# Kernel tuning notes

Measured on AMD Instinct MI355X. Metric: run time of the kernel, lower is better.

Reference implementation:

```python
import jax, jax.numpy as jnp
import numpy as np

CAPSULES = 64
CAPSULE_DIM = 32
ROUTINGS = 3
EPS = 1e-7  # K.epsilon()


def setup_inputs() -> dict:
    key = jax.random.key(0)
    k1, k2 = jax.random.split(key)
    inputs = jax.random.normal(k1, (32, 2048, 16), dtype=jnp.float32)
    # W: (capsules, input_capsules, capsule_dim, input_capsule_dim), glorot-ish scale
    W = jax.random.normal(k2, (CAPSULES, 2048, CAPSULE_DIM, 16), dtype=jnp.float32) * 0.05
    return {"inputs": inputs, "W": W}


def squash(s):
    # s: [..., capsule_dim]
    s_norm = jnp.sum(jnp.square(s), axis=-1, keepdims=True)
    scale = s_norm / (1.0 + s_norm) / jnp.sqrt(s_norm + EPS)
    return s * scale


def reference(inputs, W):
    # inputs: [b, i, j] (batch, input_capsules, input_capsule_dim)
    # W:      [c, i, d, j] (capsules, input_capsules, capsule_dim, input_capsule_dim)
    # u_hat = batched predictions: [b, c, i, d]
    u_hat = jnp.einsum('bij,cidj->bcid', inputs, W)
    B = inputs.shape[0]
    b = jnp.zeros((B, CAPSULES, u_hat.shape[2]), dtype=u_hat.dtype)
    v = None
    for r in range(ROUTINGS):
        c = jax.nn.softmax(b, axis=1)              # softmax over capsules axis
        s = jnp.einsum('bci,bcid->bcd', c, u_hat)  # weighted sum over input capsules
        v = squash(s)                              # [b, c, d]
        # Original updates b for r > 0; the update at the final iteration has no
        # effect on the output, so it is skipped for efficiency (identical math).
        if 0 < r < ROUTINGS - 1:
            b = b + jnp.einsum('bcd,bcid->bci', v, u_hat)
    return v
```

## Files before the change

### kernel.cpp

```cpp
#include <hip/hip_runtime.h>
#include <math.h>

#define B_   32
#define I_   2048
#define J_   16
#define C_   64
#define D_   32
#define CD_  2048
#define W_CSTR (I_*D_*J_)
#define W_ISTR (D_*J_)
#define X_BSTR (I_*J_)
#define EPS_ 1e-7f

typedef _Float16 half8 __attribute__((ext_vector_type(8)));
typedef float    f32x16 __attribute__((ext_vector_type(16)));


__device__ __forceinline__ half8 wfrag_from_f32(const float* __restrict__ W,
                                                int c, int i, int l) {
  const float* wp = W + (size_t)c*W_CSTR + (size_t)i*W_ISTR
                      + (size_t)(l & 31)*J_ + ((l >> 5) << 3);
  float4 a = *(const float4*)wp;
  float4 b = *(const float4*)(wp + 4);
  half8 h;
  h[0]=(_Float16)a.x; h[1]=(_Float16)a.y; h[2]=(_Float16)a.z; h[3]=(_Float16)a.w;
  h[4]=(_Float16)b.x; h[5]=(_Float16)b.y; h[6]=(_Float16)b.z; h[7]=(_Float16)b.w;
  return h;
}

__global__ __launch_bounds__(256) void k_xpack(const float* __restrict__ x,
                                               half8* __restrict__ xh) {
  const int tg = blockIdx.x*256 + threadIdx.x;
  const int i = tg >> 6, l = tg & 63;
  const int b = l & 31, jb = (l >> 5) << 3;
  const float* xp = x + (size_t)b*X_BSTR + (size_t)i*J_ + jb;
  float4 a = *(const float4*)xp;
  float4 bb = *(const float4*)(xp + 4);
  half8 h;
  h[0]=(_Float16)a.x;  h[1]=(_Float16)a.y;  h[2]=(_Float16)a.z;  h[3]=(_Float16)a.w;
  h[4]=(_Float16)bb.x; h[5]=(_Float16)bb.y; h[6]=(_Float16)bb.z; h[7]=(_Float16)bb.w;
  xh[tg] = h;
}

template<bool WRITE_WB>
__global__ __launch_bounds__(512, 4) void k_passA(const float* __restrict__ W,
                                                  const half8* __restrict__ xh,
                                                  float* __restrict__ part,
                                                  _Float16* __restrict__ WB) {
  const int t = threadIdx.x, l = t & 63, w = t >> 6;
  const int ic = blockIdx.x, c = blockIdx.y*8 + w;
  f32x16 acc = {};
  #pragma unroll 2
  for (int ii = 0; ii < 32; ii++) {
    const int i = ic*32 + ii;
    half8 wf = wfrag_from_f32(W, c, i, l);
    half8 xf = xh[(size_t)i*64 + l];
    if (WRITE_WB)
      *(half8*)(WB + ((size_t)c*I_ + i)*512 + (size_t)l*8) = wf;
    acc = __builtin_amdgcn_mfma_f32_32x32x16_f16(xf, wf, acc, 0, 0, 0);
  }
  const int col = c*32 + (l & 31), h4 = (l >> 5)*4;
  #pragma unroll
  for (int r = 0; r < 16; r++) {
    const int row = (r & 3) + 8*(r >> 2) + h4;
    part[(size_t)ic*(B_*CD_) + (size_t)row*CD_ + col] = acc[r];
  }
}

__global__ void k_reduce(const float* __restrict__ part, float* __restrict__ sfull) {
  const int g = blockIdx.x*256 + threadIdx.x;
  float s = 0.f;
  #pragma unroll 8
  for (int ch = 0; ch < 64; ch++) s += part[(size_t)ch*(B_*CD_) + g];
  sfull[g] = s;
}

__global__ void k_squash(const float* __restrict__ sfull, float* __restrict__ outp,
                         float scale) {
  const int g = blockIdx.x*256 + threadIdx.x;
  if (g >= 2048) return;
  float s[32]; float sn = 0.f;
  #pragma unroll
  for (int d = 0; d < 32; d++) {
    s[d] = sfull[(size_t)g*32 + d] * scale;
    sn += s[d]*s[d];
  }
  const float sc = sn / ((1.f + sn) * sqrtf(sn + EPS_));
  #pragma unroll
  for (int d = 0; d < 32; d++) outp[(size_t)g*32 + d] = s[d]*sc;
}

template<bool USE_WB>
__global__ __launch_bounds__(512, 4) void k_blogit(const float* __restrict__ W,
                                                   const _Float16* __restrict__ WB,
                                                   const half8* __restrict__ xh,
                                                   const float* __restrict__ v1,
                                                   float* __restrict__ b1) {
  const int t = threadIdx.x, l = t & 63, w = t >> 6;
  const int ic = blockIdx.x, c = blockIdx.y*8 + w;
  const int d = l & 31, h4 = (l >> 5)*4;

  float v1r[16];
  #pragma unroll
  for (int r = 0; r < 16; r++) {
    const int row = (r & 3) + 8*(r >> 2) + h4;
    v1r[r] = v1[((size_t)row*64 + c)*32 + d];
  }

  #pragma unroll 2
  for (int ii = 0; ii < 32; ii++) {
    const int i = ic*32 + ii;
    half8 wf = USE_WB ? *(const half8*)(WB + ((size_t)c*I_ + i)*512 + (size_t)l*8)
                      : wfrag_from_f32(W, c, i, l);
    half8 xf = xh[(size_t)i*64 + l];
    f32x16 z = {};
    f32x16 u = __builtin_amdgcn_mfma_f32_32x32x16_f16(xf, wf, z, 0, 0, 0);

    float p[16];
    #pragma unroll
    for (int r = 0; r < 16; r++) p[r] = v1r[r] * u[r];
    #pragma unroll
    for (int s = 1; s <= 16; s <<= 1) {
      #pragma unroll
      for (int r = 0; r < 16; r++) p[r] += __shfl_xor(p[r], s);
    }
    if ((l & 31) == 0) {
      float* dst = b1 + ((size_t)i*64 + c)*32 + h4;
      #pragma unroll
      for (int g = 0; g < 4; g++)
        *(float4*)(dst + 8*g) = make_float4(p[4*g], p[4*g+1], p[4*g+2], p[4*g+3]);
    }
  }
}

__global__ __launch_bounds__(256) void k_softmaxT(const float* __restrict__ b1,
                                                  float* __restrict__ c2) {
  __shared__ float ST[2048];
  __shared__ float inv[32];
  const int i = blockIdx.x, t = threadIdx.x;
  const float* src = b1 + (size_t)i*2048;
  *(float4*)(ST + t*8)     = *(const float4*)(src + t*8);
  *(float4*)(ST + t*8 + 4) = *(const float4*)(src + t*8 + 4);
  __syncthreads();
  if (t < 32) {
    float m = -1e30f;
    for (int cc = 0; cc < 64; cc++) m = fmaxf(m, ST[cc*32 + t]);
    float s = 0.f;
    for (int cc = 0; cc < 64; cc++) {
      const float e = __expf(ST[cc*32 + t] - m);
      s += e;
      ST[cc*32 + t] = e;
    }
    inv[t] = 1.f / s;
  }
  __syncthreads();
  float* dst = c2 + (size_t)i*2048;
  #pragma unroll
  for (int k = 0; k < 2; k++) {
    const int base = t*8 + k*4;
    float4 v = *(const float4*)(ST + base);
    v.x *= inv[(base+0) & 31]; v.y *= inv[(base+1) & 31];
    v.z *= inv[(base+2) & 31]; v.w *= inv[(base+3) & 31];
    *(float4*)(dst + base) = v;
  }
}

template<bool USE_WB>
__global__ __launch_bounds__(512, 4) void k_passB2(const float* __restrict__ W,
                                                   const _Float16* __restrict__ WB,
                                                   const half8* __restrict__ xh,
                                                   const float* __restrict__ c2,
                                                   float* __restrict__ part) {
  const int t = threadIdx.x, l = t & 63, w = t >> 6;
  const int ic = blockIdx.x, c = blockIdx.y*8 + w;
  const int h4 = (l >> 5)*4;
  f32x16 s2 = {};
  #pragma unroll 2
  for (int ii = 0; ii < 32; ii++) {
    const int i = ic*32 + ii;
    half8 wf = USE_WB ? *(const half8*)(WB + ((size_t)c*I_ + i)*512 + (size_t)l*8)
                      : wfrag_from_f32(W, c, i, l);
    half8 xf = xh[(size_t)i*64 + l];
    f32x16 z = {};
    f32x16 u = __builtin_amdgcn_mfma_f32_32x32x16_f16(xf, wf, z, 0, 0, 0);
    const float* cp = c2 + ((size_t)i*64 + c)*32 + h4;
    float4 c0 = *(const float4*)(cp);
    float4 c1 = *(const float4*)(cp + 8);
    float4 cB = *(const float4*)(cp + 16);
    float4 c3 = *(const float4*)(cp + 24);
    s2[0] += c0.x*u[0];  s2[1] += c0.y*u[1];  s2[2]  += c0.z*u[2];  s2[3]  += c0.w*u[3];
    s2[4] += c1.x*u[4];  s2[5] += c1.y*u[5];  s2[6]  += c1.z*u[6];  s2[7]  += c1.w*u[7];
    s2[8] += cB.x*u[8];  s2[9] += cB.y*u[9];  s2[10] += cB.z*u[10]; s2[11] += cB.w*u[11];
    s2[12]+= c3.x*u[12]; s2[13]+= c3.y*u[13]; s2[14] += c3.z*u[14]; s2[15] += c3.w*u[15];
  }
  const int col = c*32 + (l & 31);
  #pragma unroll
  for (int r = 0; r < 16; r++) {
    const int row = (r & 3) + 8*(r >> 2) + h4;
    part[(size_t)ic*(B_*CD_) + (size_t)row*CD_ + col] = s2[r];
  }
}

extern "C" void kernel_launch(void* const* d_in, const int* in_sizes, int n_in,
                              void* d_out, int out_size, void* d_ws, size_t ws_size,
                              hipStream_t stream) {
  (void)in_sizes; (void)n_in; (void)out_size;
  const float* x = (const float*)d_in[0];
  const float* W = (const float*)d_in[1];
  float* out = (float*)d_out;

  const size_t MiB = 1024*1024;
  char* ws = (char*)d_ws;
  const bool big = ws_size >= 163*MiB;

  _Float16* WB; float *part, *b1, *c2, *xhp, *sfull, *v1;
  if (big) {
    WB    = (_Float16*)(ws);
    part  = (float*)(ws + 128*MiB);
    b1    = part;
    c2    = (float*)(ws + 144*MiB);
    xhp   = (float*)(ws + 160*MiB);
    sfull = (float*)(ws + 162*MiB);
    v1    = (float*)(ws + 162*MiB + 256*1024);
  } else {
    WB    = nullptr;
    part  = (float*)(ws);
    b1    = part;
    c2    = (float*)(ws + 16*MiB);
    xhp   = (float*)(ws + 32*MiB);
    sfull = (float*)(ws + 34*MiB);
    v1    = (float*)(ws + 34*MiB + 256*1024);
  }
  half8* xh = (half8*)xhp;

  k_xpack<<<512, 256, 0, stream>>>(x, xh);
  if (big) k_passA<true ><<<dim3(64, 8), 512, 0, stream>>>(W, xh, part, WB);
  else     k_passA<false><<<dim3(64, 8), 512, 0, stream>>>(W, xh, part, WB);
  k_reduce<<<256, 256, 0, stream>>>(part, sfull);
  k_squash<<<8, 256, 0, stream>>>(sfull, v1, 1.f/64.f);
  if (big) k_blogit<true ><<<dim3(64, 8), 512, 0, stream>>>(W, WB, xh, v1, b1);
  else     k_blogit<false><<<dim3(64, 8), 512, 0, stream>>>(W, WB, xh, v1, b1);
  k_softmaxT<<<2048, 256, 0, stream>>>(b1, c2);
  if (big) k_passB2<true ><<<dim3(64, 8), 512, 0, stream>>>(W, WB, xh, c2, part);
  else     k_passB2<false><<<dim3(64, 8), 512, 0, stream>>>(W, WB, xh, c2, part);
  k_reduce<<<256, 256, 0, stream>>>(part, sfull);
  k_squash<<<8, 256, 0, stream>>>(sfull, out, 1.f);
}
```

Before: 548.9 us.

## Fuse reduce with squash, use transpose-style shuffle reduction, parallelize softmax

Merges the partial-sum reduction and the squash into one kernel, computing the squared norm with a 32-lane warp shuffle so the intermediate sfull buffer and one launch go away. Replaces the 80-shuffle butterfly in the logit kernel with a halving transpose-reduce of 31 shuffles, so each lane pair writes one output. Spreads the softmax over all 256 threads with partial max and sum in shared memory instead of using only 32 threads. Also raises the unroll factor in pass A. The added shuffle selects and the extra softmax barriers add some overhead.

```diff
diff --git a/kernel.cpp b/kernel.cpp
--- a/kernel.cpp
+++ b/kernel.cpp
@@ -50,7 +50,7 @@
   const int t = threadIdx.x, l = t & 63, w = t >> 6;
   const int ic = blockIdx.x, c = blockIdx.y*8 + w;
   f32x16 acc = {};
-  #pragma unroll 2
+  #pragma unroll 4
   for (int ii = 0; ii < 32; ii++) {
     const int i = ic*32 + ii;
     half8 wf = wfrag_from_f32(W, c, i, l);
@@ -67,27 +67,19 @@
   }
 }
 
-__global__ void k_reduce(const float* __restrict__ part, float* __restrict__ sfull) {
+__global__ __launch_bounds__(256) void k_redsquash(const float* __restrict__ part,
+                                                   float* __restrict__ outp,
+                                                   float scale) {
   const int g = blockIdx.x*256 + threadIdx.x;
   float s = 0.f;
   #pragma unroll 8
   for (int ch = 0; ch < 64; ch++) s += part[(size_t)ch*(B_*CD_) + g];
-  sfull[g] = s;
-}
-
-__global__ void k_squash(const float* __restrict__ sfull, float* __restrict__ outp,
-                         float scale) {
-  const int g = blockIdx.x*256 + threadIdx.x;
-  if (g >= 2048) return;
-  float s[32]; float sn = 0.f;
-  #pragma unroll
-  for (int d = 0; d < 32; d++) {
-    s[d] = sfull[(size_t)g*32 + d] * scale;
-    sn += s[d]*s[d];
-  }
+  s *= scale;
+  float sn = s*s;
+  #pragma unroll
+  for (int off = 1; off <= 16; off <<= 1) sn += __shfl_xor(sn, off);
   const float sc = sn / ((1.f + sn) * sqrtf(sn + EPS_));
-  #pragma unroll
-  for (int d = 0; d < 32; d++) outp[(size_t)g*32 + d] = s[d]*sc;
+  outp[g] = s*sc;
 }
 
 template<bool USE_WB>
@@ -106,6 +98,11 @@
     const int row = (r & 3) + 8*(r >> 2) + h4;
     v1r[r] = v1[((size_t)row*64 + c)*32 + d];
   }
+  const int orow = (((l >> 4) & 1) ? 8 : 0) + (((l >> 3) & 1) ? 4 : 0)
+                 + (((l >> 2) & 1) ? 2 : 0) + ((l >> 1) & 1);
+  const int wrow = (orow & 3) + 8*(orow >> 2) + h4;
+
+  const bool s4 = (l & 16), s3 = (l & 8), s2b = (l & 4), s1 = (l & 2);
 
   #pragma unroll 2
   for (int ii = 0; ii < 32; ii++) {
@@ -120,48 +117,66 @@
     #pragma unroll
     for (int r = 0; r < 16; r++) p[r] = v1r[r] * u[r];
     #pragma unroll
-    for (int s = 1; s <= 16; s <<= 1) {
-      #pragma unroll
-      for (int r = 0; r < 16; r++) p[r] += __shfl_xor(p[r], s);
-    }
-    if ((l & 31) == 0) {
-      float* dst = b1 + ((size_t)i*64 + c)*32 + h4;
-      #pragma unroll
-      for (int g = 0; g < 4; g++)
-        *(float4*)(dst + 8*g) = make_float4(p[4*g], p[4*g+1], p[4*g+2], p[4*g+3]);
-    }
+    for (int r = 0; r < 16; r++) p[r] += __shfl_xor(p[r], 16);
+    float q[8];
+    #pragma unroll
+    for (int r = 0; r < 8; r++) q[r] = s4 ? p[r+8] : p[r];
+    #pragma unroll
+    for (int r = 0; r < 8; r++) q[r] += __shfl_xor(q[r], 8);
+    float q4[4];
+    #pragma unroll
+    for (int r = 0; r < 4; r++) q4[r] = s3 ? q[r+4] : q[r];
+    #pragma unroll
+    for (int r = 0; r < 4; r++) q4[r] += __shfl_xor(q4[r], 4);
+    float q2[2];
+    #pragma unroll
+    for (int r = 0; r < 2; r++) q2[r] = s2b ? q4[r+2] : q4[r];
+    #pragma unroll
+    for (int r = 0; r < 2; r++) q2[r] += __shfl_xor(q2[r], 2);
+    float y = s1 ? q2[1] : q2[0];
+    y += __shfl_xor(y, 1);
+
+    if ((l & 1) == 0)
+      b1[((size_t)i*64 + c)*32 + wrow] = y;
   }
 }
 
 __global__ __launch_bounds__(256) void k_softmaxT(const float* __restrict__ b1,
                                                   float* __restrict__ c2) {
   __shared__ float ST[2048];
-  __shared__ float inv[32];
+  __shared__ float PM[256], PS[256];
   const int i = blockIdx.x, t = threadIdx.x;
   const float* src = b1 + (size_t)i*2048;
   *(float4*)(ST + t*8)     = *(const float4*)(src + t*8);
   *(float4*)(ST + t*8 + 4) = *(const float4*)(src + t*8 + 4);
   __syncthreads();
-  if (t < 32) {
-    float m = -1e30f;
-    for (int cc = 0; cc < 64; cc++) m = fmaxf(m, ST[cc*32 + t]);
-    float s = 0.f;
-    for (int cc = 0; cc < 64; cc++) {
-      const float e = __expf(ST[cc*32 + t] - m);
-      s += e;
-      ST[cc*32 + t] = e;
-    }
-    inv[t] = 1.f / s;
-  }
+  const int b = t & 31, ck = t >> 5;
+  float m = -1e30f;
+  #pragma unroll
+  for (int cc = 0; cc < 8; cc++) m = fmaxf(m, ST[(ck*8 + cc)*32 + b]);
+  PM[t] = m;
   __syncthreads();
+  #pragma unroll
+  for (int k = 0; k < 8; k++) m = fmaxf(m, PM[k*32 + b]);
+  float s = 0.f;
+  #pragma unroll
+  for (int cc = 0; cc < 8; cc++) {
+    const int idx = (ck*8 + cc)*32 + b;
+    const float e = __expf(ST[idx] - m);
+    s += e;
+    ST[idx] = e;
+  }
+  PS[t] = s;
+  __syncthreads();
+  s = 0.f;
+  #pragma unroll
+  for (int k = 0; k < 8; k++) s += PS[k*32 + b];
+  const float inv = 1.f / s;
   float* dst = c2 + (size_t)i*2048;
   #pragma unroll
-  for (int k = 0; k < 2; k++) {
-    const int base = t*8 + k*4;
-    float4 v = *(const float4*)(ST + base);
-    v.x *= inv[(base+0) & 31]; v.y *= inv[(base+1) & 31];
-    v.z *= inv[(base+2) & 31]; v.w *= inv[(base+3) & 31];
-    *(float4*)(dst + base) = v;
+  for (int cc = 0; cc < 8; cc++) {
+    const int idx = (ck*8 + cc)*32 + b;
+    dst[idx] = ST[idx] * inv;
   }
 }
 
@@ -213,36 +228,32 @@
   char* ws = (char*)d_ws;
   const bool big = ws_size >= 163*MiB;
 
-  _Float16* WB; float *part, *b1, *c2, *xhp, *sfull, *v1;
+  _Float16* WB; float *part, *b1, *c2, *xhp, *v1;
   if (big) {
     WB    = (_Float16*)(ws);
     part  = (float*)(ws + 128*MiB);
     b1    = part;
     c2    = (float*)(ws + 144*MiB);
     xhp   = (float*)(ws + 160*MiB);
-    sfull = (float*)(ws + 162*MiB);
-    v1    = (float*)(ws + 162*MiB + 256*1024);
+    v1    = (float*)(ws + 162*MiB);
   } else {
     WB    = nullptr;
     part  = (float*)(ws);
     b1    = part;
     c2    = (float*)(ws + 16*MiB);
     xhp   = (float*)(ws + 32*MiB);
-    sfull = (float*)(ws + 34*MiB);
-    v1    = (float*)(ws + 34*MiB + 256*1024);
+    v1    = (float*)(ws + 34*MiB);
   }
   half8* xh = (half8*)xhp;
 
   k_xpack<<<512, 256, 0, stream>>>(x, xh);
   if (big) k_passA<true ><<<dim3(64, 8), 512, 0, stream>>>(W, xh, part, WB);
   else     k_passA<false><<<dim3(64, 8), 512, 0, stream>>>(W, xh, part, WB);
-  k_reduce<<<256, 256, 0, stream>>>(part, sfull);
-  k_squash<<<8, 256, 0, stream>>>(sfull, v1, 1.f/64.f);
+  k_redsquash<<<256, 256, 0, stream>>>(part, v1, 1.f/64.f);
   if (big) k_blogit<true ><<<dim3(64, 8), 512, 0, stream>>>(W, WB, xh, v1, b1);
   else     k_blogit<false><<<dim3(64, 8), 512, 0, stream>>>(W, WB, xh, v1, b1);
   k_softmaxT<<<2048, 256, 0, stream>>>(b1, c2);
   if (big) k_passB2<true ><<<dim3(64, 8), 512, 0, stream>>>(W, WB, xh, c2, part);
   else     k_passB2<false><<<dim3(64, 8), 512, 0, stream>>>(W, WB, xh, c2, part);
-  k_reduce<<<256, 256, 0, stream>>>(part, sfull);
-  k_squash<<<8, 256, 0, stream>>>(sfull, out, 1.f);
-}
+  k_redsquash<<<256, 256, 0, stream>>>(part, out, 1.f);
+}
```

After: 541.5 us. About the same (-1.3%).
